# Kernel tuning notes

Measured on AMD Instinct MI355X. Metric: run time of the kernel, lower is better.

Reference implementation:

```python
import jax, jax.numpy as jnp
import numpy as np

NUM_EXPERTS = 16
TOP_K = 2
AUX_LOSS_WEIGHT = 0.01


def setup_inputs() -> dict:
    key = jax.random.key(0)
    k1, k2 = jax.random.split(key)
    B, H, W, D = 64, 56, 56, 512
    x = jax.random.normal(k1, (B, H, W, D), dtype=jnp.float32)
    # xavier_uniform for [E, D]
    limit = float(np.sqrt(6.0 / (NUM_EXPERTS + D)))
    expert_queries = jax.random.uniform(k2, (NUM_EXPERTS, D), dtype=jnp.float32,
                                        minval=-limit, maxval=limit)
    temperature = jnp.ones((1,), dtype=jnp.float32)
    return {"x": x, "expert_queries": expert_queries, "temperature": temperature}


def reference(x, expert_queries, temperature):
    # logits: [B, H, W, E]
    logits = jnp.einsum("bhwd,ed->bhwe", x, expert_queries) / temperature[0]
    gate_scores = jax.nn.softmax(logits, axis=-1)
    # aux load-balancing loss (training mode -> top_k)
    avg_gate_scores = gate_scores.mean(axis=(0, 1, 2))  # [E]
    flat = gate_scores.reshape(-1, NUM_EXPERTS)
    _, top_k_idx = jax.lax.top_k(flat, TOP_K)  # [N, k]
    mask = jax.nn.one_hot(top_k_idx, NUM_EXPERTS, dtype=flat.dtype).sum(axis=-2)  # [N, E]
    load = (mask / TOP_K).mean(axis=0)  # [E]
    aux_loss = AUX_LOSS_WEIGHT * (avg_gate_scores * load).mean() * (NUM_EXPERTS ** 2)
    return gate_scores, aux_loss
```

## Files before the change

### kernel.cpp

```cpp
#include <hip/hip_runtime.h>
#include <hip/hip_bf16.h>
#include <math.h>


#define NROWS 200704
#define DDIM 512
#define NEXP 16
#define KSTEPS 16
#define NTILES (NROWS / 16)
#define NBLOCKS 448
#define NWAVES (NBLOCKS * 4)

typedef __attribute__((ext_vector_type(8))) short short8;
typedef __attribute__((ext_vector_type(4))) float f32x4;

static __device__ inline short f2bf(float f) {
    __bf16 h = (__bf16)f;
    return __builtin_bit_cast(short, h);
}

static __device__ inline short8 pack8(float4 a, float4 b) {
    short8 r;
    r[0] = f2bf(a.x); r[1] = f2bf(a.y); r[2] = f2bf(a.z); r[3] = f2bf(a.w);
    r[4] = f2bf(b.x); r[5] = f2bf(b.y); r[6] = f2bf(b.z); r[7] = f2bf(b.w);
    return r;
}

__global__ __launch_bounds__(256, 2) void gate_kernel(
    const float* __restrict__ x,
    const float* __restrict__ q,
    const float* __restrict__ temp,
    float* __restrict__ out,
    float* __restrict__ ws)
{
    const int lane = threadIdx.x & 63;
    const int wid  = threadIdx.x >> 6;
    const int gwave = blockIdx.x * 4 + wid;
    const int e = lane & 15;
    const int g = lane >> 4;

    const float invT = 1.0f / temp[0];

    short8 bq[KSTEPS];
    {
        const float* qp = q + e * DDIM + g * 8;
#pragma unroll
        for (int s = 0; s < KSTEPS; ++s) {
            float4 a = *reinterpret_cast<const float4*>(qp + s * 32);
            float4 b = *reinterpret_cast<const float4*>(qp + s * 32 + 4);
            bq[s] = pack8(a, b);
        }
    }

    float sS = 0.0f;
    float sC = 0.0f;

    for (int t = gwave; t < NTILES; t += NWAVES) {
        const float* xr = x + (size_t)t * 16 * DDIM + (size_t)e * DDIM + g * 8;
        float4 a0[KSTEPS], a1[KSTEPS];
#pragma unroll
        for (int s = 0; s < KSTEPS; ++s) {
            a0[s] = *reinterpret_cast<const float4*>(xr + s * 32);
            a1[s] = *reinterpret_cast<const float4*>(xr + s * 32 + 4);
        }

        f32x4 acc = {0.0f, 0.0f, 0.0f, 0.0f};
#pragma unroll
        for (int s = 0; s < KSTEPS; ++s) {
            acc = __builtin_amdgcn_mfma_f32_16x16x32_bf16(
                pack8(a0[s], a1[s]), bq[s], acc, 0, 0, 0);
        }

#pragma unroll
        for (int r = 0; r < 4; ++r) {
            const float logit = acc[r] * invT;
            float m = logit;
            m = fmaxf(m, __shfl_xor(m, 1, 64));
            m = fmaxf(m, __shfl_xor(m, 2, 64));
            m = fmaxf(m, __shfl_xor(m, 4, 64));
            m = fmaxf(m, __shfl_xor(m, 8, 64));
            const float p = __expf(logit - m);
            float s = p;
            s += __shfl_xor(s, 1, 64);
            s += __shfl_xor(s, 2, 64);
            s += __shfl_xor(s, 4, 64);
            s += __shfl_xor(s, 8, 64);
            const float gate = p / s;

            float m2 = (logit == m) ? -3.4e38f : logit;
            m2 = fmaxf(m2, __shfl_xor(m2, 1, 64));
            m2 = fmaxf(m2, __shfl_xor(m2, 2, 64));
            m2 = fmaxf(m2, __shfl_xor(m2, 4, 64));
            m2 = fmaxf(m2, __shfl_xor(m2, 8, 64));
            const bool topk = (logit >= m2);

            const int row = t * 16 + g * 4 + r;
            out[(size_t)row * NEXP + e] = gate;
            sS += gate;
            sC += topk ? 1.0f : 0.0f;
        }
    }

    sS += __shfl_xor(sS, 16, 64); sS += __shfl_xor(sS, 32, 64);
    sC += __shfl_xor(sC, 16, 64); sC += __shfl_xor(sC, 32, 64);

    __shared__ float sred[32];
    if (threadIdx.x < 32) sred[threadIdx.x] = 0.0f;
    __syncthreads();
    if (lane < 16) {
        atomicAdd(&sred[e], sS);
        atomicAdd(&sred[16 + e], sC);
    }
    __syncthreads();
    if (threadIdx.x < 32) atomicAdd(&ws[threadIdx.x], sred[threadIdx.x]);
}

__global__ void aux_kernel(const float* __restrict__ ws, float* __restrict__ out) {
    if (threadIdx.x == 0 && blockIdx.x == 0) {
        float a = 0.0f;
#pragma unroll
        for (int e = 0; e < NEXP; ++e) a += ws[e] * ws[16 + e];
        const float n = (float)NROWS;
        out[(size_t)NROWS * NEXP] = 0.08f * a / (n * n);
    }
}

extern "C" void kernel_launch(void* const* d_in, const int* in_sizes, int n_in,
                              void* d_out, int out_size, void* d_ws, size_t ws_size,
                              hipStream_t stream) {
    const float* x = (const float*)d_in[0];
    const float* q = (const float*)d_in[1];
    const float* t = (const float*)d_in[2];
    float* out = (float*)d_out;
    float* ws = (float*)d_ws;

    hipMemsetAsync(ws, 0, 32 * sizeof(float), stream);
    gate_kernel<<<NBLOCKS, 256, 0, stream>>>(x, q, t, out, ws);
    aux_kernel<<<1, 64, 0, stream>>>(ws, out);
}
```

Measured before the change: 117.3 us.

## Swap MFMA operands, use atomic tile queue, and raise occupancy

```diff
diff --git a/kernel.cpp b/kernel.cpp
--- a/kernel.cpp
+++ b/kernel.cpp
@@ -8,8 +8,7 @@
 #define NEXP 16
 #define KSTEPS 16
 #define NTILES (NROWS / 16)
-#define NBLOCKS 448
-#define NWAVES (NBLOCKS * 4)
+#define NBLOCKS 1024
 
 typedef __attribute__((ext_vector_type(8))) short short8;
 typedef __attribute__((ext_vector_type(4))) float f32x4;
@@ -26,7 +25,7 @@
     return r;
 }
 
-__global__ __launch_bounds__(256, 2) void gate_kernel(
+__global__ __launch_bounds__(256, 4) void gate_kernel(
     const float* __restrict__ x,
     const float* __restrict__ q,
     const float* __restrict__ temp,
@@ -34,82 +33,95 @@
     float* __restrict__ ws)
 {
     const int lane = threadIdx.x & 63;
-    const int wid  = threadIdx.x >> 6;
-    const int gwave = blockIdx.x * 4 + wid;
-    const int e = lane & 15;
-    const int g = lane >> 4;
+    const int fe = lane & 15;
+    const int g  = lane >> 4;
+    int* qcnt = (int*)ws + 32;
 
     const float invT = 1.0f / temp[0];
 
-    short8 bq[KSTEPS];
+    short8 aq[KSTEPS];
     {
-        const float* qp = q + e * DDIM + g * 8;
+        const float* qp = q + fe * DDIM + g * 8;
 #pragma unroll
         for (int s = 0; s < KSTEPS; ++s) {
             float4 a = *reinterpret_cast<const float4*>(qp + s * 32);
             float4 b = *reinterpret_cast<const float4*>(qp + s * 32 + 4);
-            bq[s] = pack8(a, b);
+            aq[s] = pack8(a, b);
         }
     }
 
-    float sS = 0.0f;
-    float sC = 0.0f;
+    float sS[4] = {0, 0, 0, 0};
+    float sC[4] = {0, 0, 0, 0};
 
-    for (int t = gwave; t < NTILES; t += NWAVES) {
-        const float* xr = x + (size_t)t * 16 * DDIM + (size_t)e * DDIM + g * 8;
-        float4 a0[KSTEPS], a1[KSTEPS];
-#pragma unroll
-        for (int s = 0; s < KSTEPS; ++s) {
-            a0[s] = *reinterpret_cast<const float4*>(xr + s * 32);
-            a1[s] = *reinterpret_cast<const float4*>(xr + s * 32 + 4);
-        }
+    for (;;) {
+        int t = 0;
+        if (lane == 0) t = atomicAdd(qcnt, 1);
+        t = __shfl(t, 0, 64);
+        if (t >= NTILES) break;
 
+        const float* xr = x + (size_t)t * 16 * DDIM + (size_t)fe * DDIM + g * 8;
         f32x4 acc = {0.0f, 0.0f, 0.0f, 0.0f};
 #pragma unroll
         for (int s = 0; s < KSTEPS; ++s) {
-            acc = __builtin_amdgcn_mfma_f32_16x16x32_bf16(
-                pack8(a0[s], a1[s]), bq[s], acc, 0, 0, 0);
+            float4 a = *reinterpret_cast<const float4*>(xr + s * 32);
+            float4 b = *reinterpret_cast<const float4*>(xr + s * 32 + 4);
+            acc = __builtin_amdgcn_mfma_f32_16x16x32_bf16(aq[s], pack8(a, b),
+                                                          acc, 0, 0, 0);
         }
 
-#pragma unroll
-        for (int r = 0; r < 4; ++r) {
-            const float logit = acc[r] * invT;
-            float m = logit;
-            m = fmaxf(m, __shfl_xor(m, 1, 64));
-            m = fmaxf(m, __shfl_xor(m, 2, 64));
-            m = fmaxf(m, __shfl_xor(m, 4, 64));
-            m = fmaxf(m, __shfl_xor(m, 8, 64));
-            const float p = __expf(logit - m);
-            float s = p;
-            s += __shfl_xor(s, 1, 64);
-            s += __shfl_xor(s, 2, 64);
-            s += __shfl_xor(s, 4, 64);
-            s += __shfl_xor(s, 8, 64);
-            const float gate = p / s;
+        const float l0 = acc[0] * invT, l1 = acc[1] * invT;
+        const float l2 = acc[2] * invT, l3 = acc[3] * invT;
 
-            float m2 = (logit == m) ? -3.4e38f : logit;
-            m2 = fmaxf(m2, __shfl_xor(m2, 1, 64));
-            m2 = fmaxf(m2, __shfl_xor(m2, 2, 64));
-            m2 = fmaxf(m2, __shfl_xor(m2, 4, 64));
-            m2 = fmaxf(m2, __shfl_xor(m2, 8, 64));
-            const bool topk = (logit >= m2);
+        float m = fmaxf(fmaxf(l0, l1), fmaxf(l2, l3));
+        m = fmaxf(m, __shfl_xor(m, 16, 64));
+        m = fmaxf(m, __shfl_xor(m, 32, 64));
 
-            const int row = t * 16 + g * 4 + r;
-            out[(size_t)row * NEXP + e] = gate;
-            sS += gate;
-            sC += topk ? 1.0f : 0.0f;
-        }
+        const float p0 = __expf(l0 - m), p1 = __expf(l1 - m);
+        const float p2 = __expf(l2 - m), p3 = __expf(l3 - m);
+        float s4 = (p0 + p1) + (p2 + p3);
+        s4 += __shfl_xor(s4, 16, 64);
+        s4 += __shfl_xor(s4, 32, 64);
+        const float inv = 1.0f / s4;
+        const float g0 = p0 * inv, g1 = p1 * inv, g2 = p2 * inv, g3 = p3 * inv;
+
+        const float NI = -3.4e38f;
+        const float M0 = (l0 == m) ? NI : l0, M1 = (l1 == m) ? NI : l1;
+        const float M2 = (l2 == m) ? NI : l2, M3 = (l3 == m) ? NI : l3;
+        float m2 = fmaxf(fmaxf(M0, M1), fmaxf(M2, M3));
+        m2 = fmaxf(m2, __shfl_xor(m2, 16, 64));
+        m2 = fmaxf(m2, __shfl_xor(m2, 32, 64));
+
+        sS[0] += g0; sS[1] += g1; sS[2] += g2; sS[3] += g3;
+        sC[0] += (l0 >= m2) ? 1.0f : 0.0f;
+        sC[1] += (l1 >= m2) ? 1.0f : 0.0f;
+        sC[2] += (l2 >= m2) ? 1.0f : 0.0f;
+        sC[3] += (l3 >= m2) ? 1.0f : 0.0f;
+
+        float4 o = make_float4(g0, g1, g2, g3);
+        *reinterpret_cast<float4*>(out + ((size_t)t * 16 + fe) * NEXP + g * 4) = o;
     }
 
-    sS += __shfl_xor(sS, 16, 64); sS += __shfl_xor(sS, 32, 64);
-    sC += __shfl_xor(sC, 16, 64); sC += __shfl_xor(sC, 32, 64);
+#pragma unroll
+    for (int r = 0; r < 4; ++r) {
+        sS[r] += __shfl_xor(sS[r], 1, 64);
+        sS[r] += __shfl_xor(sS[r], 2, 64);
+        sS[r] += __shfl_xor(sS[r], 4, 64);
+        sS[r] += __shfl_xor(sS[r], 8, 64);
+        sC[r] += __shfl_xor(sC[r], 1, 64);
+        sC[r] += __shfl_xor(sC[r], 2, 64);
+        sC[r] += __shfl_xor(sC[r], 4, 64);
+        sC[r] += __shfl_xor(sC[r], 8, 64);
+    }
 
     __shared__ float sred[32];
     if (threadIdx.x < 32) sred[threadIdx.x] = 0.0f;
     __syncthreads();
-    if (lane < 16) {
-        atomicAdd(&sred[e], sS);
-        atomicAdd(&sred[16 + e], sC);
+    if (fe == 0) {
+#pragma unroll
+        for (int r = 0; r < 4; ++r) {
+            atomicAdd(&sred[g * 4 + r], sS[r]);
+            atomicAdd(&sred[16 + g * 4 + r], sC[r]);
+        }
     }
     __syncthreads();
     if (threadIdx.x < 32) atomicAdd(&ws[threadIdx.x], sred[threadIdx.x]);
@@ -134,7 +146,7 @@
     float* out = (float*)d_out;
     float* ws = (float*)d_ws;
 
-    hipMemsetAsync(ws, 0, 32 * sizeof(float), stream);
+    hipMemsetAsync(ws, 0, 33 * sizeof(float), stream);
     gate_kernel<<<NBLOCKS, 256, 0, stream>>>(x, q, t, out, ws);
     aux_kernel<<<1, 64, 0, stream>>>(ws, out);
 }
```

Result: slower. 224.9 us (+91.8%).
